# Performance work log

Measured on AMD Instinct MI355X. Metric: run time of the kernel, lower is better.

## Reference

```python
import jax, jax.numpy as jnp
import numpy as np

B, S, E, H, W = 4, 2048, 1024, 16, 512  # batch, seq, embed, heads, sliding window
D = E // H
NB = S // W  # number of query blocks
SCALE = 1.0 / np.sqrt(D)  # flex_attention default scale applied BEFORE score_mod
START_TOKEN = 0


def setup_inputs() -> dict:
    key = jax.random.key(0)
    k1, k2, k3 = jax.random.split(key, 3)
    x = jax.random.normal(k1, (B, S, E), jnp.float32)
    w_in = jax.random.normal(k2, (3 * E, E), jnp.float32) * 0.02   # packed qkv, Linear(E,3E,bias=False)
    w_out = jax.random.normal(k3, (E, E), jnp.float32) * 0.02      # Linear(E,E,bias=False)
    return {"x": x, "w_in": w_in, "w_out": w_out}


def _attn(x, w_in, w_out):
    # packed in-projection: proj.unflatten(-1,(3,E)) -> q,k,v
    proj = x @ w_in.T                                   # [B,S,3E]
    q, k, v = jnp.split(proj, 3, axis=-1)
    to_heads = lambda t: t.reshape(B, S, H, D).transpose(0, 2, 1, 3)  # [B,H,S,D]
    q, k, v = to_heads(q), to_heads(k), to_heads(v)

    # honor sliding-window sparsity: each query block of size W attends only
    # to its own block and the previous block (q_idx>=kv_idx & q_idx-kv_idx<W)
    qb = q.reshape(B, H, NB, W, D)
    kb = k.reshape(B, H, NB, W, D)
    vb = v.reshape(B, H, NB, W, D)
    pad = jnp.zeros((B, H, 1, W, D), q.dtype)
    k2 = jnp.concatenate([jnp.concatenate([pad, kb[:, :, :-1]], axis=2), kb], axis=3)  # [B,H,NB,2W,D]
    v2 = jnp.concatenate([jnp.concatenate([pad, vb[:, :, :-1]], axis=2), vb], axis=3)

    scores = jnp.einsum('bhnqd,bhnkd->bhnqk', qb, k2) * SCALE        # [B,H,NB,W,2W]

    # relative position q_idx - kv_idx (same for every block by construction)
    qi = jnp.arange(W)[:, None]
    ki = jnp.arange(2 * W)[None, :]
    rel = qi + W - ki                                                # [W,2W]

    # ALiBi: score + (q_idx + start_token - kv_idx) * exp2(-(h+1)*8/H)  (code ADDS bias)
    slopes = jnp.exp2(-(jnp.arange(1, H + 1, dtype=jnp.float32) * 8.0 / H))  # [H]
    bias = (rel.astype(jnp.float32) + START_TOKEN)[None, :, :] * slopes[:, None, None]  # [H,W,2W]
    scores = scores + bias[None, :, None, :, :]

    # causal + sliding window mask, and invalidate the zero-padded block before block 0
    win_mask = (rel >= 0) & (rel < W)                                # [W,2W]
    blk = jnp.arange(NB)[:, None, None]
    kv_valid = (blk >= 1) | (ki[None, :, :] >= W)                    # [NB,1,2W]
    mask = win_mask[None, :, :] & kv_valid                           # [NB,W,2W]
    scores = jnp.where(mask[None, None], scores, -jnp.inf)

    p = jax.nn.softmax(scores, axis=-1)
    o = jnp.einsum('bhnqk,bhnkd->bhnqd', p, v2).reshape(B, H, S, D)
    o = o.transpose(0, 2, 1, 3).reshape(B, S, E)
    return o @ w_out.T                                               # [B,S,E]


def reference(x, w_in, w_out):
    return _attn(x, w_in, w_out)
```

## Files before the change

kernel.cpp:

```cpp
#include <hip/hip_runtime.h>

typedef unsigned short ushort_t;
typedef __attribute__((ext_vector_type(8))) __bf16 bf16x8;
typedef __attribute__((ext_vector_type(4))) float f32x4;

#define EXP2F(x) __builtin_amdgcn_exp2f(x)
#define LOG2E 1.44269504088896340736f


__device__ __forceinline__ ushort_t f2bf(float f) {
  unsigned u = __float_as_uint(f);
  u += 0x7fffu + ((u >> 16) & 1u);
  return (ushort_t)(u >> 16);
}

__device__ __forceinline__ f32x4 mfma16(bf16x8 a, bf16x8 b, f32x4 c) {
  return __builtin_amdgcn_mfma_f32_16x16x32_bf16(a, b, c, 0, 0, 0);
}

__device__ __forceinline__ void gload16(const ushort_t* g, ushort_t* l) {
  __builtin_amdgcn_global_load_lds((__attribute__((address_space(1))) void*)g,
                                   (__attribute__((address_space(3))) void*)l,
                                   16, 0, 0);
}

__global__ __launch_bounds__(256) void cast_two(const float* __restrict__ a,
                                                ushort_t* __restrict__ oa, int na,
                                                const float* __restrict__ b,
                                                ushort_t* __restrict__ ob, int nb) {
  int i = (blockIdx.x * 256 + threadIdx.x) * 4;
  if (i < na) {
    float4 v = *(const float4*)(a + i);
    ushort4 o;
    o.x = f2bf(v.x); o.y = f2bf(v.y); o.z = f2bf(v.z); o.w = f2bf(v.w);
    *(ushort4*)(oa + i) = o;
  } else {
    int j = i - na;
    if (j < nb) {
      float4 v = *(const float4*)(b + j);
      ushort4 o;
      o.x = f2bf(v.x); o.y = f2bf(v.y); o.z = f2bf(v.z); o.w = f2bf(v.w);
      *(ushort4*)(ob + j) = o;
    }
  }
}

__global__ __launch_bounds__(256) void cast_f32_bf16(const float* __restrict__ in,
                                                     ushort_t* __restrict__ out, int n) {
  int i = (blockIdx.x * 256 + threadIdx.x) * 4;
  if (i < n) {
    float4 v = *(const float4*)(in + i);
    ushort4 o;
    o.x = f2bf(v.x); o.y = f2bf(v.y); o.z = f2bf(v.z); o.w = f2bf(v.w);
    *(ushort4*)(out + i) = o;
  }
}

template <bool C_F32>
__global__ __launch_bounds__(256) void gemm_bt(const ushort_t* __restrict__ A,
                                               const ushort_t* __restrict__ Bt,
                                               void* __restrict__ Cp,
                                               int N, int K, int ldA) {
  __shared__ ushort_t As[128 * 64];
  __shared__ ushort_t Bs[128 * 64];
  const int tid = threadIdx.x;
  const int wave = tid >> 6;
  const int lane = tid & 63;
  const int g = lane >> 4;
  const int q = lane & 15;
  const int qm = q & 7;
  const int row0 = blockIdx.y * 128;
  const int col0 = blockIdx.x * 128;
  const int wm = (wave >> 1) * 64;
  const int wn = (wave & 1) * 64;

  const f32x4 fzero = {0.f, 0.f, 0.f, 0.f};
  f32x4 acc[4][4];
#pragma unroll
  for (int i = 0; i < 4; ++i)
#pragma unroll
    for (int j = 0; j < 4; ++j) acc[i][j] = fzero;

  const int rs = tid >> 3;
  const int cs = (((tid & 7) ^ (rs & 7)) << 3);
  const ushort_t* ag = A + (size_t)(row0 + rs) * ldA + cs;
  const ushort_t* bg = Bt + (size_t)(col0 + rs) * K + cs;
  ushort_t* lA = As + (size_t)(wave * 64 + lane) * 8;
  ushort_t* lB = Bs + (size_t)(wave * 64 + lane) * 8;

  const int sw0 = ((g ^ qm) << 3);
  const int sw1 = (((4 + g) ^ qm) << 3);

  for (int kt = 0; kt < K; kt += 64) {
    __syncthreads();
#pragma unroll
    for (int u = 0; u < 4; ++u) {
      gload16(ag + (size_t)(u * 32) * ldA + kt, lA + u * 2048);
      gload16(bg + (size_t)(u * 32) * K + kt, lB + u * 2048);
    }
    __syncthreads();
#pragma unroll
    for (int ks = 0; ks < 2; ++ks) {
      const int sw = ks ? sw1 : sw0;
      bf16x8 af[4], bfv[4];
#pragma unroll
      for (int mi = 0; mi < 4; ++mi)
        af[mi] = *(const bf16x8*)(As + (wm + mi * 16 + q) * 64 + sw);
#pragma unroll
      for (int ni = 0; ni < 4; ++ni)
        bfv[ni] = *(const bf16x8*)(Bs + (wn + ni * 16 + q) * 64 + sw);
      __builtin_amdgcn_s_setprio(1);
#pragma unroll
      for (int mi = 0; mi < 4; ++mi)
#pragma unroll
        for (int ni = 0; ni < 4; ++ni)
          acc[mi][ni] = mfma16(af[mi], bfv[ni], acc[mi][ni]);
      __builtin_amdgcn_s_setprio(0);
    }
  }

#pragma unroll
  for (int mi = 0; mi < 4; ++mi)
#pragma unroll
    for (int ni = 0; ni < 4; ++ni)
#pragma unroll
      for (int r = 0; r < 4; ++r) {
        size_t rr = (size_t)(row0 + wm + mi * 16 + 4 * g + r);
        size_t cc = (size_t)(col0 + wn + ni * 16 + q);
        if (C_F32) ((float*)Cp)[rr * N + cc] = acc[mi][ni][r];
        else ((ushort_t*)Cp)[rr * N + cc] = f2bf(acc[mi][ni][r]);
      }
}

__global__ __launch_bounds__(256) void transpose_v(const ushort_t* __restrict__ proj,
                                                   ushort_t* __restrict__ Vt) {
  __shared__ ushort_t tile[64][80];
  const int t = threadIdx.x;
  const int bh = blockIdx.x;
  const int s0 = blockIdx.y * 64;
  const int b = bh >> 4;
  const int h = bh & 15;
  {
    const int r = t >> 3;
    const int c = (t & 7) * 8;
#pragma unroll
    for (int i = 0; i < 2; ++i) {
      int row = i * 32 + r;
      const ushort_t* src = proj + (size_t)(b * 2048 + s0 + row) * 3072 + 2048 + h * 64 + c;
      *(uint4*)(&tile[row][c]) = *(const uint4*)(src);
    }
  }
  __syncthreads();
  {
    const int d = t >> 2;
    const int sc = (t & 3) * 16;
    union { ushort_t u[16]; uint4 v[2]; } tmp;
#pragma unroll
    for (int j = 0; j < 16; ++j) {
      int col = sc + j;
      int s = col & 31;
      int g2 = s >> 3, jj = s & 7;
      int src_key = (col & ~31) + ((jj < 4) ? (4 * g2 + jj) : (16 + 4 * g2 + (jj - 4)));
      tmp.u[j] = tile[src_key][d];
    }
    ushort_t* dst = Vt + ((size_t)bh * 64 + d) * 2048 + s0 + sc;
    *(uint4*)(dst) = tmp.v[0];
    *(uint4*)(dst + 8) = tmp.v[1];
  }
}

__global__ __launch_bounds__(512, 4) void attn_kernel(const ushort_t* __restrict__ proj,
                                                      const ushort_t* __restrict__ Vt,
                                                      ushort_t* __restrict__ attn_out,
                                                      int ostride) {
  __shared__ ushort_t Ks[2][4096];
  __shared__ ushort_t Vs[2][4096];
  const int tid = threadIdx.x;
  const int wave = tid >> 6;
  const int lane = tid & 63;
  const int g = lane >> 4;
  const int q = lane & 15;
  const int bid = blockIdx.x;
  const int xcd = bid & 7;
  const int j = bid >> 3;
  const int bh = xcd * 8 + (j >> 4);
  const int tile = j & 15;
  const int b = bh >> 4;
  const int h = bh & 15;
  const int q0b = tile * 128;
  const int qw0 = q0b + wave * 16;
  const int qglob = qw0 + q;

  const float slope2 = EXP2F(-(float)(h + 1) * 0.5f) * LOG2E;
  const float sc2 = 0.125f * LOG2E;

  const ushort_t* qptr = proj + (size_t)(b * 2048 + qglob) * 3072 + h * 64 + g * 8;
  const bf16x8 qa0 = *(const bf16x8*)(qptr);
  const bf16x8 qa1 = *(const bf16x8*)(qptr + 32);

  const int r0 = tid >> 3;
  const int c0s = (((tid & 7) ^ (r0 & 7)) << 3);
  const ushort_t* kgb = proj + (size_t)(b * 2048) * 3072 + 1024 + h * 64;
  const ushort_t* vgb = Vt + (size_t)(bh * 64) * 2048;

  const int qm = q & 7;
  const int sw0 = ((g ^ qm) << 3);
  const int sw1 = (((g + 4) ^ qm) << 3);

  const f32x4 fzero = {0.f, 0.f, 0.f, 0.f};
  f32x4 acc[4];
#pragma unroll
  for (int t2 = 0; t2 < 4; ++t2) acc[t2] = fzero;
  float m2 = -1e30f;
  float lsum = 0.f;
  const int relbase = qglob - 4 * g;

  int kc_lo = q0b - 512;
  if (kc_lo < 0) kc_lo = 0;
  const int nch = ((q0b + 127 - kc_lo) >> 6) + 1;

#define STAGE(bi, kcv)                                                        \
  gload16(kgb + (size_t)((kcv) + r0) * 3072 + c0s, &Ks[bi][(size_t)tid * 8]); \
  gload16(vgb + (size_t)r0 * 2048 + (kcv) + c0s, &Vs[bi][(size_t)tid * 8]);

  STAGE(0, kc_lo)
  __syncthreads();

  for (int c = 0; c < nch; ++c) {
    const int kc = kc_lo + (c << 6);
    const ushort_t* Kb = Ks[c & 1];
    const ushort_t* Vb = Vs[c & 1];
    if (c + 1 < nch) { STAGE((c + 1) & 1, kc + 64) }

    if (kc <= qw0 + 15 && kc >= qw0 - 574) {
      const int rbi = relbase - kc;
      float p[16];
      float mc = -1e30f;

      if (kc >= qw0 - 496 && kc <= qw0 - 63) {
        const float bb = (float)rbi * slope2;
        __builtin_amdgcn_s_setprio(1);
#pragma unroll
        for (int i = 0; i < 4; ++i) {
          const int row = (i << 4) + q;
          bf16x8 ka = *(const bf16x8*)(Kb + row * 64 + sw0);
          bf16x8 kb = *(const bf16x8*)(Kb + row * 64 + sw1);
          f32x4 si = mfma16(kb, qa1, mfma16(ka, qa0, fzero));
#pragma unroll
          for (int r = 0; r < 4; ++r) {
            float sc = fmaf(si[r], sc2, bb) - (float)((i << 4) + r) * slope2;
            p[(i << 2) + r] = sc;
            mc = fmaxf(mc, sc);
          }
        }
        __builtin_amdgcn_s_setprio(0);
      } else {
        __builtin_amdgcn_s_setprio(1);
#pragma unroll
        for (int i = 0; i < 4; ++i) {
          const int row = (i << 4) + q;
          bf16x8 ka = *(const bf16x8*)(Kb + row * 64 + sw0);
          bf16x8 kb = *(const bf16x8*)(Kb + row * 64 + sw1);
          f32x4 si = mfma16(kb, qa1, mfma16(ka, qa0, fzero));
#pragma unroll
          for (int r = 0; r < 4; ++r) {
            const int rel = rbi - ((i << 4) + r);
            float sc = ((unsigned)rel < 512u) ? fmaf(si[r], sc2, (float)rel * slope2)
                                              : -1e30f;
            p[(i << 2) + r] = sc;
            mc = fmaxf(mc, sc);
          }
        }
        __builtin_amdgcn_s_setprio(0);
      }

      if (__any(mc > m2 + 8.f)) {
        float mg = fmaxf(mc, m2);
        mg = fmaxf(mg, __shfl_xor(mg, 16, 64));
        mg = fmaxf(mg, __shfl_xor(mg, 32, 64));
        const float factor = EXP2F(m2 - mg);
        lsum *= factor;
#pragma unroll
        for (int t2 = 0; t2 < 4; ++t2) acc[t2] *= factor;
        m2 = mg;
      }
#pragma unroll
      for (int i = 0; i < 16; ++i) p[i] = EXP2F(p[i] - m2);
      float ps0 = (p[0] + p[1]) + (p[2] + p[3]);
      float ps1 = (p[4] + p[5]) + (p[6] + p[7]);
      float ps2 = (p[8] + p[9]) + (p[10] + p[11]);
      float ps3 = (p[12] + p[13]) + (p[14] + p[15]);
      lsum += (ps0 + ps1) + (ps2 + ps3);

      bf16x8 pv0, pv1;
#pragma unroll
      for (int r = 0; r < 4; ++r) {
        pv0[r] = (__bf16)p[r];       pv0[4 + r] = (__bf16)p[4 + r];
        pv1[r] = (__bf16)p[8 + r];   pv1[4 + r] = (__bf16)p[12 + r];
      }

      __builtin_amdgcn_s_setprio(1);
#pragma unroll
      for (int t2 = 0; t2 < 4; ++t2) {
        const int d = (t2 << 4) + q;
        bf16x8 vf0 = *(const bf16x8*)(Vb + d * 64 + sw0);
        bf16x8 vf1 = *(const bf16x8*)(Vb + d * 64 + sw1);
        acc[t2] = mfma16(vf0, pv0, acc[t2]);
        acc[t2] = mfma16(vf1, pv1, acc[t2]);
      }
      __builtin_amdgcn_s_setprio(0);
    }

    __syncthreads();
  }
#undef STAGE

  lsum += __shfl_xor(lsum, 16, 64);
  lsum += __shfl_xor(lsum, 32, 64);
  const float inv = 1.f / lsum;

  ushort_t* ob = attn_out + (size_t)(b * 2048 + qglob) * ostride + h * 64;
#pragma unroll
  for (int t2 = 0; t2 < 4; ++t2)
#pragma unroll
    for (int r = 0; r < 4; ++r)
      ob[16 * t2 + 4 * g + r] = f2bf(acc[t2][r] * inv);
}

extern "C" void kernel_launch(void* const* d_in, const int* in_sizes, int n_in,
                              void* d_out, int out_size, void* d_ws, size_t ws_size,
                              hipStream_t stream) {
  const float* x = nullptr;
  const float* w_in = nullptr;
  const float* w_out = nullptr;
  for (int i = 0; i < n_in; ++i) {
    if (in_sizes[i] == 8388608) x = (const float*)d_in[i];
    else if (in_sizes[i] == 3145728) w_in = (const float*)d_in[i];
    else if (in_sizes[i] == 1048576) w_out = (const float*)d_in[i];
  }
  if (!(x && w_in && w_out)) { x = (const float*)d_in[0]; w_in = (const float*)d_in[1]; w_out = (const float*)d_in[2]; }

  char* ws = (char*)d_ws;
  ushort_t* proj = (ushort_t*)(ws);
  ushort_t* xb   = (ushort_t*)(ws + (size_t)50331648);
  ushort_t* Vt   = xb;
  ushort_t* wob  = xb;
  ushort_t* wib  = (ushort_t*)d_out;

  cast_two<<<11264, 256, 0, stream>>>(x, xb, 8388608, w_in, wib, 3145728);
  gemm_bt<false><<<dim3(24, 64), 256, 0, stream>>>(xb, wib, proj, 3072, 1024, 1024);
  transpose_v<<<dim3(64, 32), 256, 0, stream>>>(proj, Vt);
  attn_kernel<<<1024, 512, 0, stream>>>(proj, Vt, proj + 2048, 3072);
  cast_f32_bf16<<<1024, 256, 0, stream>>>(w_out, wob, 1048576);
  gemm_bt<true><<<dim3(8, 64), 256, 0, stream>>>(proj + 2048, wob, d_out, 1024, 1024, 3072);
}
```

Before: 149.0 us.

## Fuse V transpose into QKV GEMM epilogue and raise attention occupancy

The QKV projection GEMM now writes V tiles straight into the transposed, key-permuted Vt layout from its epilogue, which removes the separate transpose_v kernel and its extra read and write of V. Vt moves into spare space in the output buffer so the w_out cast can run before attention. The attention kernel's launch bounds go from 4 to 8 waves-per-EU minimum, which may force register spills. The fused epilogue writes 8-byte ushort4 stores that are strided across rows, which may coalesce less well than before.

```diff
diff --git a/kernel.cpp b/kernel.cpp
--- a/kernel.cpp
+++ b/kernel.cpp
@@ -56,10 +56,11 @@
   }
 }
 
-template <bool C_F32>
+template <bool C_F32, bool FUSE_V>
 __global__ __launch_bounds__(256) void gemm_bt(const ushort_t* __restrict__ A,
                                                const ushort_t* __restrict__ Bt,
                                                void* __restrict__ Cp,
+                                               ushort_t* __restrict__ Vt,
                                                int N, int K, int ldA) {
   __shared__ ushort_t As[128 * 64];
   __shared__ ushort_t Bs[128 * 64];
@@ -119,57 +120,39 @@
     }
   }
 
-#pragma unroll
-  for (int mi = 0; mi < 4; ++mi)
-#pragma unroll
-    for (int ni = 0; ni < 4; ++ni)
-#pragma unroll
-      for (int r = 0; r < 4; ++r) {
-        size_t rr = (size_t)(row0 + wm + mi * 16 + 4 * g + r);
-        size_t cc = (size_t)(col0 + wn + ni * 16 + q);
-        if (C_F32) ((float*)Cp)[rr * N + cc] = acc[mi][ni][r];
-        else ((ushort_t*)Cp)[rr * N + cc] = f2bf(acc[mi][ni][r]);
-      }
-}
-
-__global__ __launch_bounds__(256) void transpose_v(const ushort_t* __restrict__ proj,
-                                                   ushort_t* __restrict__ Vt) {
-  __shared__ ushort_t tile[64][80];
-  const int t = threadIdx.x;
-  const int bh = blockIdx.x;
-  const int s0 = blockIdx.y * 64;
-  const int b = bh >> 4;
-  const int h = bh & 15;
-  {
-    const int r = t >> 3;
-    const int c = (t & 7) * 8;
-#pragma unroll
-    for (int i = 0; i < 2; ++i) {
-      int row = i * 32 + r;
-      const ushort_t* src = proj + (size_t)(b * 2048 + s0 + row) * 3072 + 2048 + h * 64 + c;
-      *(uint4*)(&tile[row][c]) = *(const uint4*)(src);
-    }
-  }
-  __syncthreads();
-  {
-    const int d = t >> 2;
-    const int sc = (t & 3) * 16;
-    union { ushort_t u[16]; uint4 v[2]; } tmp;
-#pragma unroll
-    for (int j = 0; j < 16; ++j) {
-      int col = sc + j;
-      int s = col & 31;
-      int g2 = s >> 3, jj = s & 7;
-      int src_key = (col & ~31) + ((jj < 4) ? (4 * g2 + jj) : (16 + 4 * g2 + (jj - 4)));
-      tmp.u[j] = tile[src_key][d];
-    }
-    ushort_t* dst = Vt + ((size_t)bh * 64 + d) * 2048 + s0 + sc;
-    *(uint4*)(dst) = tmp.v[0];
-    *(uint4*)(dst + 8) = tmp.v[1];
-  }
-}
-
-__global__ __launch_bounds__(512, 4) void attn_kernel(const ushort_t* __restrict__ proj,
+  if (FUSE_V && col0 >= 2048) {
+#pragma unroll
+    for (int mi = 0; mi < 4; ++mi) {
+      const int rr = row0 + wm + mi * 16 + 4 * g;
+      const int bb = rr >> 11;
+      const int pbase = ((rr & 2047) & ~31) + 8 * g + 4 * (mi & 1);
+#pragma unroll
+      for (int ni = 0; ni < 4; ++ni) {
+        const int cc = col0 + wn + ni * 16 + q - 2048;
+        const int bh = bb * 16 + (cc >> 6);
+        const int dd = cc & 63;
+        ushort4 o;
+        o.x = f2bf(acc[mi][ni][0]); o.y = f2bf(acc[mi][ni][1]);
+        o.z = f2bf(acc[mi][ni][2]); o.w = f2bf(acc[mi][ni][3]);
+        *(ushort4*)(Vt + (size_t)(bh * 64 + dd) * 2048 + pbase) = o;
+      }
+    }
+  } else {
+#pragma unroll
+    for (int mi = 0; mi < 4; ++mi)
+#pragma unroll
+      for (int ni = 0; ni < 4; ++ni)
+#pragma unroll
+        for (int r = 0; r < 4; ++r) {
+          size_t rr = (size_t)(row0 + wm + mi * 16 + 4 * g + r);
+          size_t cc = (size_t)(col0 + wn + ni * 16 + q);
+          if (C_F32) ((float*)Cp)[rr * N + cc] = acc[mi][ni][r];
+          else ((ushort_t*)Cp)[rr * N + cc] = f2bf(acc[mi][ni][r]);
+        }
+  }
+}
+
+__global__ __launch_bounds__(512, 8) void attn_kernel(const ushort_t* __restrict__ proj,
                                                       const ushort_t* __restrict__ Vt,
                                                       ushort_t* __restrict__ attn_out,
                                                       int ostride) {
@@ -343,14 +326,13 @@
   char* ws = (char*)d_ws;
   ushort_t* proj = (ushort_t*)(ws);
   ushort_t* xb   = (ushort_t*)(ws + (size_t)50331648);
-  ushort_t* Vt   = xb;
   ushort_t* wob  = xb;
   ushort_t* wib  = (ushort_t*)d_out;
+  ushort_t* Vt   = (ushort_t*)((char*)d_out + (size_t)8388608);
 
   cast_two<<<11264, 256, 0, stream>>>(x, xb, 8388608, w_in, wib, 3145728);
-  gemm_bt<false><<<dim3(24, 64), 256, 0, stream>>>(xb, wib, proj, 3072, 1024, 1024);
-  transpose_v<<<dim3(64, 32), 256, 0, stream>>>(proj, Vt);
+  gemm_bt<false, true><<<dim3(24, 64), 256, 0, stream>>>(xb, wib, proj, Vt, 3072, 1024, 1024);
+  cast_f32_bf16<<<1024, 256, 0, stream>>>(w_out, wob, 1048576);
   attn_kernel<<<1024, 512, 0, stream>>>(proj, Vt, proj + 2048, 3072);
-  cast_f32_bf16<<<1024, 256, 0, stream>>>(w_out, wob, 1048576);
-  gemm_bt<true><<<dim3(8, 64), 256, 0, stream>>>(proj + 2048, wob, d_out, 1024, 1024, 3072);
-}
+  gemm_bt<true, false><<<dim3(8, 64), 256, 0, stream>>>(proj + 2048, wob, d_out, nullptr, 1024, 1024, 3072);
+}
```

New measurement: 189.3 us. +27.0%, slower.
